# Optimization experiments

Measured on AMD Instinct MI355X. Metric: run time of the kernel, lower is better.

## Reference

```python
import jax, jax.numpy as jnp
import numpy as np

N, C, O, R, T, V = 128, 64, 64, 8, 128, 25  # batch, in_ch, out_ch, rel_ch, frames, joints
EPS = 1e-5


def _c1(x, w, b):
    # 1x1 conv2d over channel dim: x [n,i,t,v], w [o,i], b [o]
    return jnp.einsum('oi,nitv->notv', w, x) + b[None, :, None, None]


def _tconv(x, w):
    # temporal conv, kernel [3,1], pad [1,0]: x [n,c,t,1], w [o,i,3,1]
    return jax.lax.conv_general_dilated(
        x, w, window_strides=(1, 1), padding=((1, 1), (0, 0)),
        dimension_numbers=('NCHW', 'OIHW', 'NCHW'))


def setup_inputs() -> dict:
    key = jax.random.key(0)
    ks = jax.random.split(key, 16)
    d = {}
    d['x'] = jax.random.normal(ks[0], (N, C, T, V), jnp.float32)
    d['A'] = jax.random.normal(ks[1], (V, V), jnp.float32) * 0.1
    d['alpha'] = jnp.ones((1,), jnp.float32)
    s_c = 1.0 / np.sqrt(C)
    s_r = 1.0 / np.sqrt(R)
    d['w1'] = jax.random.normal(ks[2], (R, C), jnp.float32) * s_c
    d['b1'] = jnp.zeros((R,), jnp.float32)
    d['w2'] = jax.random.normal(ks[3], (R, C), jnp.float32) * s_c
    d['b2'] = jnp.zeros((R,), jnp.float32)
    d['w5'] = jax.random.normal(ks[4], (R, C), jnp.float32) * s_c
    d['b5'] = jnp.zeros((R,), jnp.float32)
    d['w3'] = jax.random.normal(ks[5], (O, R), jnp.float32) * s_r
    d['b3'] = jnp.zeros((O,), jnp.float32)
    d['w4'] = jax.random.normal(ks[6], (O, R), jnp.float32) * s_r
    d['b4'] = jnp.zeros((O,), jnp.float32)
    # RouteFuncMLP params (ratio=1, kernels=[3,3])
    d['g_w'] = jax.random.normal(ks[7], (R, R), jnp.float32) * s_r
    d['g_b'] = jnp.zeros((R,), jnp.float32)
    d['a_w'] = jax.random.normal(ks[8], (R, R, 3, 1), jnp.float32) * s_r
    d['a_b'] = jnp.zeros((R,), jnp.float32)
    d['bn_g'] = jnp.ones((R,), jnp.float32)
    d['bn_b'] = jnp.zeros((R,), jnp.float32)
    d['bn_rm'] = jnp.zeros((R,), jnp.float32)
    d['bn_rv'] = jnp.ones((R,), jnp.float32)
    # conv_rf.b is zero-init in torch (trivial gate); randomize small for a meaningful test
    d['rf_bw'] = jax.random.normal(ks[9], (R, R, 3, 1), jnp.float32) * 0.05
    return d


def reference(x, A, alpha, w1, b1, w2, b2, w5, b5, w3, b3, w4, b4,
              g_w, g_b, a_w, a_b, bn_g, bn_b, bn_rm, bn_rv, rf_bw):
    # x1, x2: 1x1 conv then mean over T  -> [N,R,V]
    x1 = _c1(x, w1, b1).mean(axis=2)
    x2 = _c1(x, w2, b2).mean(axis=2)
    x3 = _c1(x, w5, b5)  # [N,R,T,V]

    # RouteFuncMLP gating on x3
    g = x3.mean(axis=(2, 3), keepdims=True)          # global pool [N,R,1,1]
    p = x3.mean(axis=3, keepdims=True)               # pool over V [N,R,T,1]
    gg = _c1(g, g_w, g_b)                            # 1x1 conv on global pool
    h = _tconv(p + gg, a_w) + a_b[None, :, None, None]
    h = (h - bn_rm[None, :, None, None]) * (bn_g / jnp.sqrt(bn_rv + EPS))[None, :, None, None] + bn_b[None, :, None, None]
    h = jax.nn.relu(h)
    rf = _tconv(h, rf_bw) + 1.0                      # [N,R,T,1]

    x3 = _c1(x3 * rf, w3, b3)                        # [N,O,T,V]

    # relation tensor: broadcast diff + tanh -> [N,R,V,V]
    rel = jnp.tanh(x1[:, :, :, None] - x2[:, :, None, :])
    rel = _c1(rel, w4, b4) * alpha[0] + A[None, None]  # [N,O,V,V]

    # aggregation: out[n,c,t,u] = sum_v rel[n,c,u,v] * x3[n,c,t,v]
    out = jnp.einsum('ncuv,nctv->nctu', rel, x3)
    return out
```

## Files before the change

kernel.cpp:

```cpp
#include <hip/hip_runtime.h>

#define N_ 128
#define C_ 64
#define O_ 64
#define R_ 8
#define T_ 128
#define V_ 25
#define TV_ 3200
#define EPS_ 1e-5f
#define G_ 8

__global__ __launch_bounds__(256) void kA(const float* __restrict__ x,
        const float* __restrict__ w5, const float* __restrict__ b5,
        const float* __restrict__ w1, const float* __restrict__ w2,
        float* __restrict__ x3, float* __restrict__ x12p, float* __restrict__ ppool) {
    int n = blockIdx.x, y = blockIdx.y;
    int tid = threadIdx.x;
    bool act = tid < 200;
    int g = tid / 25, v = tid % 25;
    __shared__ __align__(16) float wls[C_][24];
    __shared__ float ppart[R_][16];
    __shared__ float s12part[16][25];
    for (int idx = tid; idx < C_ * 24; idx += 256) {
        int i = idx / 24, r = idx % 24;
        wls[i][r] = (r < 8) ? w5[r * C_ + i]
                  : (r < 16) ? w1[(r - 8) * C_ + i]
                             : w2[(r - 16) * C_ + i];
    }
    for (int idx = tid; idx < R_ * 16; idx += 256) (&ppart[0][0])[idx] = 0.f;
    for (int idx = tid; idx < 16 * 25; idx += 256) (&s12part[0][0])[idx] = 0.f;
    __syncthreads();

    float acc0[R_], acc1[R_], s12[16];
    #pragma unroll
    for (int r = 0; r < R_; ++r) { acc0[r] = 0.f; acc1[r] = 0.f; }
    #pragma unroll
    for (int rr = 0; rr < 16; ++rr) s12[rr] = 0.f;

    if (act) {
        int off0 = (g + 16 * y) * 25 + v;
        const float* xp = x + (size_t)n * C_ * TV_;
        #pragma unroll 2
        for (int i = 0; i < C_; ++i) {
            float xv0 = xp[(size_t)i * TV_ + off0];
            float xv1 = xp[(size_t)i * TV_ + off0 + 200];
            const float4* wp = (const float4*)&wls[i][0];
            float4 q0 = wp[0], q1 = wp[1];
            float4 q2 = wp[2], q3 = wp[3];
            float4 q4 = wp[4], q5 = wp[5];
            acc0[0] += q0.x * xv0; acc0[1] += q0.y * xv0; acc0[2] += q0.z * xv0; acc0[3] += q0.w * xv0;
            acc0[4] += q1.x * xv0; acc0[5] += q1.y * xv0; acc0[6] += q1.z * xv0; acc0[7] += q1.w * xv0;
            acc1[0] += q0.x * xv1; acc1[1] += q0.y * xv1; acc1[2] += q0.z * xv1; acc1[3] += q0.w * xv1;
            acc1[4] += q1.x * xv1; acc1[5] += q1.y * xv1; acc1[6] += q1.z * xv1; acc1[7] += q1.w * xv1;
            float xs = xv0 + xv1;
            s12[0]  += q2.x * xs; s12[1]  += q2.y * xs; s12[2]  += q2.z * xs; s12[3]  += q2.w * xs;
            s12[4]  += q3.x * xs; s12[5]  += q3.y * xs; s12[6]  += q3.z * xs; s12[7]  += q3.w * xs;
            s12[8]  += q4.x * xs; s12[9]  += q4.y * xs; s12[10] += q4.z * xs; s12[11] += q4.w * xs;
            s12[12] += q5.x * xs; s12[13] += q5.y * xs; s12[14] += q5.z * xs; s12[15] += q5.w * xs;
        }
        float* x3p = x3 + (size_t)n * R_ * TV_;
        #pragma unroll
        for (int r = 0; r < R_; ++r) {
            float v0 = acc0[r] + b5[r];
            float v1 = acc1[r] + b5[r];
            x3p[(size_t)r * TV_ + off0]       = v0;
            x3p[(size_t)r * TV_ + off0 + 200] = v1;
            atomicAdd(&ppart[r][g], v0);
            atomicAdd(&ppart[r][g + 8], v1);
        }
        #pragma unroll
        for (int rr = 0; rr < 16; ++rr) atomicAdd(&s12part[rr][v], s12[rr]);
    }
    __syncthreads();
    if (tid < 128) {
        int r = tid / 16, tl = tid % 16;
        ppool[((size_t)n * R_ + r) * T_ + 16 * y + tl] = ppart[r][tl];
    }
    for (int idx = tid; idx < 400; idx += 256)
        x12p[((size_t)n * 8 + y) * 400 + idx] = (&s12part[0][0])[idx];
}

__global__ __launch_bounds__(256) void kB(const float* __restrict__ x12p,
        const float* __restrict__ b1, const float* __restrict__ b2,
        const float* __restrict__ w4, const float* __restrict__ b4,
        const float* __restrict__ A, const float* __restrict__ alpha,
        const float* __restrict__ ppool,
        const float* __restrict__ g_w, const float* __restrict__ g_b,
        const float* __restrict__ a_w, const float* __restrict__ a_b,
        const float* __restrict__ bn_g, const float* __restrict__ bn_b,
        const float* __restrict__ bn_rm, const float* __restrict__ bn_rv,
        const float* __restrict__ rf_bw,
        float* __restrict__ rel2, float* __restrict__ rf) {
    int n = blockIdx.x, tid = threadIdx.x;
    if (blockIdx.y == 4) {
        __shared__ float ps[R_][T_];
        __shared__ float hsx[R_][T_ + 2];
        __shared__ float gs[R_], ggs[R_];
        for (int idx = tid; idx < R_ * T_; idx += 256)
            ps[idx / T_][idx % T_] = ppool[(size_t)n * R_ * T_ + idx] * (1.0f / V_);
        if (tid < R_ * 2) {
            int r = tid / 2;
            hsx[r][(tid % 2) * (T_ + 1)] = 0.f;
        }
        __syncthreads();
        if (tid < R_) {
            float s = 0.f;
            for (int t = 0; t < T_; ++t) s += ps[tid][t];
            gs[tid] = s * (1.0f / T_);
        }
        __syncthreads();
        if (tid < R_) {
            float a = g_b[tid];
            #pragma unroll
            for (int i = 0; i < R_; ++i) a += g_w[tid * R_ + i] * gs[i];
            ggs[tid] = a;
        }
        __syncthreads();
        for (int idx = tid; idx < R_ * T_; idx += 256) {
            int r = idx / T_, t = idx % T_;
            float acc = a_b[r];
            #pragma unroll
            for (int i = 0; i < R_; ++i) {
                #pragma unroll
                for (int k = 0; k < 3; ++k) {
                    int tt = t + k - 1;
                    if (tt >= 0 && tt < T_)
                        acc += a_w[(r * R_ + i) * 3 + k] * (ps[i][tt] + ggs[i]);
                }
            }
            float sc = bn_g[r] * rsqrtf(bn_rv[r] + EPS_);
            hsx[r][t + 1] = fmaxf((acc - bn_rm[r]) * sc + bn_b[r], 0.f);
        }
        __syncthreads();
        for (int idx = tid; idx < R_ * T_; idx += 256) {
            int r = idx / T_, t = idx % T_;
            float acc = 1.0f;
            #pragma unroll
            for (int i = 0; i < R_; ++i) {
                #pragma unroll
                for (int k = 0; k < 3; ++k)
                    acc += rf_bw[(r * R_ + i) * 3 + k] * hsx[i][t + k];
            }
            rf[((size_t)n * R_ + r) * T_ + t] = acc;
        }
        return;
    }
    int c0 = blockIdx.y * 16;
    __shared__ float x1s[R_ * V_];
    __shared__ float x2s[R_ * V_];
    __shared__ float rels[R_ * 625];
    const float invT = 1.0f / (float)T_;
    for (int idx = tid; idx < 400; idx += 256) {
        int rr = idx / 25;
        float a = 0.f;
        #pragma unroll
        for (int b = 0; b < 8; ++b) a += x12p[((size_t)n * 8 + b) * 400 + idx];
        a = a * invT + ((rr < 8) ? b1[rr] : b2[rr - 8]);
        if (rr < 8) x1s[idx] = a; else x2s[idx - 200] = a;
    }
    __syncthreads();
    for (int idx = tid; idx < R_ * 625; idx += 256) {
        int r = idx / 625, uv = idx % 625;
        rels[idx] = tanhf(x1s[r * V_ + uv / V_] - x2s[r * V_ + uv % V_]);
    }
    __syncthreads();
    float al = alpha[0];
    for (int idx = tid; idx < 16 * 625; idx += 256) {
        int o = c0 + idx / 625, uv = idx % 625;
        float acc = b4[o];
        #pragma unroll
        for (int r = 0; r < R_; ++r) acc += w4[o * R_ + r] * rels[r * 625 + uv];
        rel2[((size_t)n * O_ + o) * 625 + uv] = acc * al + A[uv];
    }
}

__global__ __launch_bounds__(512) void k5_out(const float* __restrict__ x3,
        const float* __restrict__ rf, const float* __restrict__ rel2,
        const float* __restrict__ w3, const float* __restrict__ b3,
        float* __restrict__ out) {
    int b = blockIdx.x;
    int xcd = b & 7, slot = b >> 3;
    int n = (slot >> 4) * 8 + xcd;
    int rem = slot & 15;
    int cg = rem >> 1, th = rem & 1;
    int c0 = cg * G_;
    int tid = threadIdx.x;
    __shared__ float rfs[R_][64];
    __shared__ __align__(16) float zs[G_][1600];
    {
        int r = tid / 64, tl = tid % 64;
        rfs[r][tl] = rf[((size_t)n * R_ + r) * T_ + th * 64 + tl];
    }
    __syncthreads();
    const float* x3p = x3 + (size_t)n * R_ * TV_ + th * 1600;
    for (int p = tid; p < 1600; p += 512) {
        int t = p / V_;
        float y[R_];
        #pragma unroll
        for (int r = 0; r < R_; ++r) y[r] = x3p[(size_t)r * TV_ + p] * rfs[r][t];
        #pragma unroll
        for (int cl = 0; cl < G_; ++cl) {
            float a = b3[c0 + cl];
            #pragma unroll
            for (int r = 0; r < R_; ++r) a += w3[(c0 + cl) * R_ + r] * y[r];
            zs[cl][p] = a;
        }
    }
    __syncthreads();
    {
        int cl = __builtin_amdgcn_readfirstlane(tid >> 6);
        int tl = tid & 63;
        const float* relp = rel2 + ((size_t)n * O_ + c0 + cl) * 625;
        float zreg[V_];
        #pragma unroll
        for (int v = 0; v < V_; ++v) zreg[v] = zs[cl][tl * V_ + v];
        float accu[V_];
        #pragma unroll
        for (int u = 0; u < V_; ++u) {
            float acc = 0.f;
            #pragma unroll
            for (int j = 0; j < V_; ++j) acc += relp[u * V_ + j] * zreg[j];
            accu[u] = acc;
        }
        #pragma unroll
        for (int u = 0; u < V_; ++u) zs[cl][tl * V_ + u] = accu[u];
    }
    __syncthreads();
    size_t ob = (((size_t)n * O_ + c0) * T_ + th * 64) * V_;
    float4* out4 = (float4*)(out + ob);
    const float4* zf4 = (const float4*)&zs[0][0];
    for (int j = tid; j < 3200; j += 512) {
        int cl = j / 400, r4 = j % 400;
        out4[(size_t)cl * 800 + r4] = zf4[j];
    }
}

extern "C" void kernel_launch(void* const* d_in, const int* in_sizes, int n_in,
                              void* d_out, int out_size, void* d_ws, size_t ws_size,
                              hipStream_t stream) {
    const float* x     = (const float*)d_in[0];
    const float* A     = (const float*)d_in[1];
    const float* alpha = (const float*)d_in[2];
    const float* w1    = (const float*)d_in[3];
    const float* b1    = (const float*)d_in[4];
    const float* w2    = (const float*)d_in[5];
    const float* b2    = (const float*)d_in[6];
    const float* w5    = (const float*)d_in[7];
    const float* b5    = (const float*)d_in[8];
    const float* w3    = (const float*)d_in[9];
    const float* b3    = (const float*)d_in[10];
    const float* w4    = (const float*)d_in[11];
    const float* b4    = (const float*)d_in[12];
    const float* g_w   = (const float*)d_in[13];
    const float* g_b   = (const float*)d_in[14];
    const float* a_w   = (const float*)d_in[15];
    const float* a_b   = (const float*)d_in[16];
    const float* bn_g  = (const float*)d_in[17];
    const float* bn_b  = (const float*)d_in[18];
    const float* bn_rm = (const float*)d_in[19];
    const float* bn_rv = (const float*)d_in[20];
    const float* rf_bw = (const float*)d_in[21];
    float* out = (float*)d_out;
    float* ws  = (float*)d_ws;

    float* x3    = ws;
    float* x12p  = x3 + 3276800;
    float* ppool = x12p + 409600;
    float* rf    = ppool + 131072;
    float* rel2  = rf + 131072;

    hipLaunchKernelGGL(kA, dim3(N_, 8), dim3(256), 0, stream,
                       x, w5, b5, w1, w2, x3, x12p, ppool);
    hipLaunchKernelGGL(kB, dim3(N_, 5), dim3(256), 0, stream,
                       x12p, b1, b2, w4, b4, A, alpha,
                       ppool, g_w, g_b, a_w, a_b, bn_g, bn_b, bn_rm, bn_rv, rf_bw,
                       rel2, rf);
    hipLaunchKernelGGL(k5_out, dim3(N_ * 16), dim3(512), 0, stream,
                       x3, rf, rel2, w3, b3, out);
}
```

Before: 318.2 us.

## Split kA over 16 time chunks, drop LDS weights and atomics, remove XCD remap

kA now handles one time row per thread over 16 chunks per sample instead of 8. Weights are read directly from global/constant memory rather than staged in LDS. The shared-memory atomic reductions are replaced by plain buffer writes followed by a serial reduction. The x12 partial-sum buffer doubles and kB sums 16 partials. k5_out's XCD-aware block-to-sample mapping is replaced with a plain linear mapping, which may hurt L2 locality of x3/rel2 across chiplets.

```diff
diff --git a/kernel.cpp b/kernel.cpp
--- a/kernel.cpp
+++ b/kernel.cpp
@@ -16,68 +16,54 @@
         float* __restrict__ x3, float* __restrict__ x12p, float* __restrict__ ppool) {
     int n = blockIdx.x, y = blockIdx.y;
     int tid = threadIdx.x;
+    int g = tid / 25, v = tid % 25;
     bool act = tid < 200;
-    int g = tid / 25, v = tid % 25;
-    __shared__ __align__(16) float wls[C_][24];
-    __shared__ float ppart[R_][16];
-    __shared__ float s12part[16][25];
-    for (int idx = tid; idx < C_ * 24; idx += 256) {
-        int i = idx / 24, r = idx % 24;
-        wls[i][r] = (r < 8) ? w5[r * C_ + i]
-                  : (r < 16) ? w1[(r - 8) * C_ + i]
-                             : w2[(r - 16) * C_ + i];
-    }
-    for (int idx = tid; idx < R_ * 16; idx += 256) (&ppart[0][0])[idx] = 0.f;
-    for (int idx = tid; idx < 16 * 25; idx += 256) (&s12part[0][0])[idx] = 0.f;
-    __syncthreads();
-
-    float acc0[R_], acc1[R_], s12[16];
+    __shared__ float x3buf[R_][8][25];
+    __shared__ float s12full[8][16 * 25];
+
+    float acc[R_], s12[16];
     #pragma unroll
-    for (int r = 0; r < R_; ++r) { acc0[r] = 0.f; acc1[r] = 0.f; }
+    for (int r = 0; r < R_; ++r) acc[r] = 0.f;
     #pragma unroll
     for (int rr = 0; rr < 16; ++rr) s12[rr] = 0.f;
 
     if (act) {
-        int off0 = (g + 16 * y) * 25 + v;
-        const float* xp = x + (size_t)n * C_ * TV_;
-        #pragma unroll 2
+        int off = (8 * y + g) * 25 + v;
+        const float* xp = x + (size_t)n * C_ * TV_ + off;
+        #pragma unroll 4
         for (int i = 0; i < C_; ++i) {
-            float xv0 = xp[(size_t)i * TV_ + off0];
-            float xv1 = xp[(size_t)i * TV_ + off0 + 200];
-            const float4* wp = (const float4*)&wls[i][0];
-            float4 q0 = wp[0], q1 = wp[1];
-            float4 q2 = wp[2], q3 = wp[3];
-            float4 q4 = wp[4], q5 = wp[5];
-            acc0[0] += q0.x * xv0; acc0[1] += q0.y * xv0; acc0[2] += q0.z * xv0; acc0[3] += q0.w * xv0;
-            acc0[4] += q1.x * xv0; acc0[5] += q1.y * xv0; acc0[6] += q1.z * xv0; acc0[7] += q1.w * xv0;
-            acc1[0] += q0.x * xv1; acc1[1] += q0.y * xv1; acc1[2] += q0.z * xv1; acc1[3] += q0.w * xv1;
-            acc1[4] += q1.x * xv1; acc1[5] += q1.y * xv1; acc1[6] += q1.z * xv1; acc1[7] += q1.w * xv1;
-            float xs = xv0 + xv1;
-            s12[0]  += q2.x * xs; s12[1]  += q2.y * xs; s12[2]  += q2.z * xs; s12[3]  += q2.w * xs;
-            s12[4]  += q3.x * xs; s12[5]  += q3.y * xs; s12[6]  += q3.z * xs; s12[7]  += q3.w * xs;
-            s12[8]  += q4.x * xs; s12[9]  += q4.y * xs; s12[10] += q4.z * xs; s12[11] += q4.w * xs;
-            s12[12] += q5.x * xs; s12[13] += q5.y * xs; s12[14] += q5.z * xs; s12[15] += q5.w * xs;
-        }
-        float* x3p = x3 + (size_t)n * R_ * TV_;
+            float xv = xp[(size_t)i * TV_];
+            #pragma unroll
+            for (int r = 0; r < R_; ++r) acc[r]     += w5[r * C_ + i] * xv;
+            #pragma unroll
+            for (int r = 0; r < R_; ++r) s12[r]     += w1[r * C_ + i] * xv;
+            #pragma unroll
+            for (int r = 0; r < R_; ++r) s12[r + 8] += w2[r * C_ + i] * xv;
+        }
+        float* x3p = x3 + (size_t)n * R_ * TV_ + (8 * y + g) * 25 + v;
         #pragma unroll
         for (int r = 0; r < R_; ++r) {
-            float v0 = acc0[r] + b5[r];
-            float v1 = acc1[r] + b5[r];
-            x3p[(size_t)r * TV_ + off0]       = v0;
-            x3p[(size_t)r * TV_ + off0 + 200] = v1;
-            atomicAdd(&ppart[r][g], v0);
-            atomicAdd(&ppart[r][g + 8], v1);
-        }
-        #pragma unroll
-        for (int rr = 0; rr < 16; ++rr) atomicAdd(&s12part[rr][v], s12[rr]);
-    }
-    __syncthreads();
-    if (tid < 128) {
-        int r = tid / 16, tl = tid % 16;
-        ppool[((size_t)n * R_ + r) * T_ + 16 * y + tl] = ppart[r][tl];
-    }
-    for (int idx = tid; idx < 400; idx += 256)
-        x12p[((size_t)n * 8 + y) * 400 + idx] = (&s12part[0][0])[idx];
+            float val = acc[r] + b5[r];
+            x3p[(size_t)r * TV_] = val;
+            x3buf[r][g][v] = val;
+        }
+        #pragma unroll
+        for (int rr = 0; rr < 16; ++rr) s12full[g][rr * 25 + v] = s12[rr];
+    }
+    __syncthreads();
+    if (tid < 64) {
+        int r = tid / 8, tl = tid % 8;
+        float s = 0.f;
+        #pragma unroll
+        for (int vv = 0; vv < V_; ++vv) s += x3buf[r][tl][vv];
+        ppool[((size_t)n * R_ + r) * T_ + 8 * y + tl] = s;
+    }
+    for (int idx = tid; idx < 400; idx += 256) {
+        float s = 0.f;
+        #pragma unroll
+        for (int gg = 0; gg < 8; ++gg) s += s12full[gg][idx];
+        x12p[((size_t)n * 16 + y) * 400 + idx] = s;
+    }
 }
 
 __global__ __launch_bounds__(256) void kB(const float* __restrict__ x12p,
@@ -154,7 +140,7 @@
         int rr = idx / 25;
         float a = 0.f;
         #pragma unroll
-        for (int b = 0; b < 8; ++b) a += x12p[((size_t)n * 8 + b) * 400 + idx];
+        for (int b = 0; b < 16; ++b) a += x12p[((size_t)n * 16 + b) * 400 + idx];
         a = a * invT + ((rr < 8) ? b1[rr] : b2[rr - 8]);
         if (rr < 8) x1s[idx] = a; else x2s[idx - 200] = a;
     }
@@ -179,10 +165,9 @@
         const float* __restrict__ w3, const float* __restrict__ b3,
         float* __restrict__ out) {
     int b = blockIdx.x;
-    int xcd = b & 7, slot = b >> 3;
-    int n = (slot >> 4) * 8 + xcd;
-    int rem = slot & 15;
-    int cg = rem >> 1, th = rem & 1;
+    int n = b / 16;
+    int rem = b % 16;
+    int cg = rem / 2, th = rem % 2;
     int c0 = cg * G_;
     int tid = threadIdx.x;
     __shared__ float rfs[R_][64];
@@ -265,11 +250,11 @@
 
     float* x3    = ws;
     float* x12p  = x3 + 3276800;
-    float* ppool = x12p + 409600;
+    float* ppool = x12p + 819200;
     float* rf    = ppool + 131072;
     float* rel2  = rf + 131072;
 
-    hipLaunchKernelGGL(kA, dim3(N_, 8), dim3(256), 0, stream,
+    hipLaunchKernelGGL(kA, dim3(N_, 16), dim3(256), 0, stream,
                        x, w5, b5, w1, w2, x3, x12p, ppool);
     hipLaunchKernelGGL(kB, dim3(N_, 5), dim3(256), 0, stream,
                        x12p, b1, b2, w4, b4, A, alpha,
```

Measured after the change: 306.3 us. 1.04x faster.
